# Kernel optimization log

Measured on AMD Instinct MI355X. Metric: run time of the kernel, lower is better.

## Reference

```python
import jax, jax.numpy as jnp
import numpy as np

B, N, NFEAT, NHID, NOUT, H = 16, 1024, 128, 256, 256, 4
DH = NOUT // H  # 64 per head
EPS = 1e-5
ALPHA = 0.2  # LeakyReLU negative slope


def setup_inputs() -> dict:
    key = jax.random.key(0)
    ks = jax.random.split(key, 8)
    stdv = 1.0 / np.sqrt(NHID)
    return {
        "x": jax.random.normal(ks[0], (B, N, NFEAT), dtype=jnp.float32),
        "adj": jax.random.uniform(ks[1], (N, N), dtype=jnp.float32) / N,
        "gc_w": jax.random.uniform(ks[2], (NFEAT, NHID), minval=-stdv, maxval=stdv, dtype=jnp.float32),
        "gc_b": jax.random.uniform(ks[3], (NHID,), minval=-stdv, maxval=stdv, dtype=jnp.float32),
        "bn1_gamma": jnp.ones((NHID,), jnp.float32),
        "bn1_beta": jnp.zeros((NHID,), jnp.float32),
        "gat_w": jax.random.normal(ks[4], (H, NHID, DH), dtype=jnp.float32) * (1.0 / np.sqrt(NHID)),
        "conv_w": jax.random.normal(ks[5], (NOUT, NOUT, 3), dtype=jnp.float32) * (1.0 / np.sqrt(NOUT * 3)),
        "conv_b": jnp.zeros((NOUT,), jnp.float32),
        "bn2_gamma": jnp.ones((NOUT,), jnp.float32),
        "bn2_beta": jnp.zeros((NOUT,), jnp.float32),
    }


def reference(x, adj, gc_w, gc_b, bn1_gamma, bn1_beta, gat_w, conv_w, conv_b, bn2_gamma, bn2_beta):
    # --- GraphConvolution: adj @ (x @ W) + b, relu ---
    h = jnp.einsum("bnf,fo->bno", x, gc_w)
    h = jnp.einsum("nm,bmo->bno", adj, h) + gc_b
    h = jax.nn.relu(h)
    # --- BatchNorm1d over channel dim (training-mode batch stats), relu ---
    mu = h.mean((0, 1))
    var = h.var((0, 1))
    h = (h - mu) * jax.lax.rsqrt(var + EPS) * bn1_gamma + bn1_beta
    h = jax.nn.relu(h)
    # --- Multi-head GAT: per head hp, e = hp hp^T, leakyrelu, softmax, attn @ hp ---
    hp = jnp.einsum("bnf,hfd->bhnd", h, gat_w)          # (B,H,N,DH)
    e = jnp.einsum("bhnd,bhmd->bhnm", hp, hp)            # (B,H,N,N)
    e = jnp.where(e > 0, e, ALPHA * e)
    attn = jax.nn.softmax(e, axis=-1)
    out = jnp.einsum("bhnm,bhmd->bhnd", attn, hp)        # = sum_m attn * hp (the B,N,N,d repeat in torch)
    out = out.transpose(0, 2, 1, 3).reshape(B, N, H * DH)  # concat heads -> (B,N,NOUT)
    # --- TCN block: conv1d (k=3, pad 1) over node axis, batchnorm, relu (dropout=eval) ---
    xc = out.transpose(0, 2, 1)                          # (B,C,N)
    y = jax.lax.conv_general_dilated(xc, conv_w, (1,), [(1, 1)],
                                     dimension_numbers=("NCH", "OIH", "NCH"))
    y = y + conv_b[None, :, None]
    mu2 = y.mean((0, 2), keepdims=True)
    var2 = y.var((0, 2), keepdims=True)
    y = (y - mu2) * jax.lax.rsqrt(var2 + EPS) * bn2_gamma[None, :, None] + bn2_beta[None, :, None]
    y = jax.nn.relu(y)
    return y.transpose(0, 2, 1)                          # (B,N,NOUT)
```

## Files before the change

kernel.cpp:

```cpp
#include <hip/hip_runtime.h>
#include <hip/hip_bf16.h>


typedef unsigned short u16;
typedef __attribute__((ext_vector_type(8))) short short8;
typedef __attribute__((ext_vector_type(4))) float f32x4;

static __device__ __forceinline__ float4 ld4(const float* p){ return *(const float4*)p; }
static __device__ __forceinline__ void st4(float* p, float4 v){ *(float4*)p = v; }

static __device__ __forceinline__ u16 f2bf(float f){
  unsigned u = __builtin_bit_cast(unsigned, f);
  unsigned r = u + 0x7FFFu + ((u >> 16) & 1u);
  return (u16)(r >> 16);
}
static __device__ __forceinline__ float bf2f(u16 h){
  unsigned u = ((unsigned)h) << 16; return __builtin_bit_cast(float, u);
}
static __device__ __forceinline__ void st4bf(u16* p, u16 a, u16 b, u16 c, u16 d){
  uint2 v; v.x = (unsigned)a | ((unsigned)b << 16); v.y = (unsigned)c | ((unsigned)d << 16);
  *(uint2*)p = v;
}
static __device__ __forceinline__ f32x4 mfma16(short8 a, short8 b, f32x4 c){
  return __builtin_amdgcn_mfma_f32_16x16x32_bf16(a, b, c, 0, 0, 0);
}

template<int SPLIT, int K, int NN, int MODE, int AXSWAP, int BM, int BN, int WR, int WC>
static __device__ __forceinline__ void mgemm_body(
    const u16* __restrict__ Ah_, const u16* __restrict__ Al_,
    const u16* __restrict__ Bh_, const u16* __restrict__ Bl_,
    const u16* __restrict__ zbuf,
    void* __restrict__ C0v, void* __restrict__ C1v, void* __restrict__ C2v,
    const float* __restrict__ bias)
{
  constexpr int KT = K / 32;
  constexpr int WM = BM / WR, WN = BN / WC;
  constexpr int MI = WM / 16, NJ = WN / 16;
  __shared__ u16 Ah[2][BM * 32], Bh[2][BN * 32];
  __shared__ u16 Al[2][SPLIT == 3 ? BM * 32 : 8], Bl[2][SPLIT == 3 ? BN * 32 : 8];
  const int tid = threadIdx.x;
  const int n0 = (AXSWAP ? blockIdx.y : blockIdx.x) * BN;
  const int m0 = (AXSWAP ? blockIdx.x : blockIdx.y) * BM;
  const int lane = tid & 63, l15 = lane & 15, lq = lane >> 4;
  const int w = tid >> 6, wr = w / WC, wc = w % WC;

  f32x4 acc[MI][NJ] = {};

  auto STAGE = [&](int buf, int kt){
    const int k0 = kt * 32;
#pragma unroll
    for (int r = 0; r < BM / 64; ++r){
      const int slot = r * 256 + tid;
      const int row = slot & (BM - 1), kh = slot / BM;
      const int ldsoff = (r * 256 + (tid & 192)) * 8;
      const u16* asrc;
      if constexpr (MODE == 3){
        const int kz = k0 >> 8;
        const int ci0 = (k0 & 255) + kh * 8;
        const int R = m0 + row;
        const int nn = (R & 1023) + kz - 1;
        asrc = ((unsigned)nn < 1024u) ? (Ah_ + (size_t)(R + kz - 1) * 256 + ci0) : zbuf;
      } else {
        asrc = Ah_ + (size_t)(m0 + row) * K + k0 + kh * 8;
      }
      __builtin_amdgcn_global_load_lds(asrc, &Ah[buf][ldsoff], 16, 0, 0);
      if constexpr (SPLIT == 3){
        const u16* asrc2 = Al_ + (size_t)(m0 + row) * K + k0 + kh * 8;
        __builtin_amdgcn_global_load_lds(asrc2, &Al[buf][ldsoff], 16, 0, 0);
      }
    }
#pragma unroll
    for (int r = 0; r < BN / 64; ++r){
      const int slot = r * 256 + tid;
      const int row = slot & (BN - 1), kh = slot / BN;
      const int ldsoff = (r * 256 + (tid & 192)) * 8;
      const u16* bsrc = Bh_ + (size_t)(n0 + row) * K + k0 + kh * 8;
      __builtin_amdgcn_global_load_lds(bsrc, &Bh[buf][ldsoff], 16, 0, 0);
      if constexpr (SPLIT == 3){
        const u16* bsrc2 = Bl_ + (size_t)(n0 + row) * K + k0 + kh * 8;
        __builtin_amdgcn_global_load_lds(bsrc2, &Bl[buf][ldsoff], 16, 0, 0);
      }
    }
  };

  STAGE(0, 0);
  __syncthreads();
  for (int kt = 0; kt < KT; ++kt){
    const int cur = kt & 1;
    if (kt + 1 < KT) STAGE(cur ^ 1, kt + 1);
    short8 afh[MI], bfh[NJ], afl[MI], bfl[NJ];
#pragma unroll
    for (int f = 0; f < MI; ++f){
      afh[f] = *(const short8*)&Ah[cur][(lq * BM + wr * WM + f * 16 + l15) * 8];
      if constexpr (SPLIT == 3)
        afl[f] = *(const short8*)&Al[cur][(lq * BM + wr * WM + f * 16 + l15) * 8];
    }
#pragma unroll
    for (int f = 0; f < NJ; ++f){
      bfh[f] = *(const short8*)&Bh[cur][(lq * BN + wc * WN + f * 16 + l15) * 8];
      if constexpr (SPLIT == 3)
        bfl[f] = *(const short8*)&Bl[cur][(lq * BN + wc * WN + f * 16 + l15) * 8];
    }
#pragma unroll
    for (int fi = 0; fi < MI; ++fi)
#pragma unroll
      for (int fj = 0; fj < NJ; ++fj){
        acc[fi][fj] = mfma16(afh[fi], bfh[fj], acc[fi][fj]);
        if constexpr (SPLIT == 3){
          acc[fi][fj] = mfma16(afl[fi], bfh[fj], acc[fi][fj]);
          acc[fi][fj] = mfma16(afh[fi], bfl[fj], acc[fi][fj]);
        }
      }
    __syncthreads();
  }

  const int rb = m0 + wr * WM;
  const int cb = n0 + wc * WN;
  if constexpr (MODE == 0){
    u16* H = (u16*)C0v; u16* L = (u16*)C1v;
#pragma unroll
    for (int fi = 0; fi < MI; ++fi){
      const int R = rb + fi * 16 + lq * 4;
      const int nn = R & 1023, bq = R >> 10;
#pragma unroll
      for (int fj = 0; fj < NJ; ++fj){
        const int c = cb + fj * 16 + l15;
        const size_t off = (size_t)(bq * 256 + c) * 1024 + nn;
        u16 h_[4], l_[4];
#pragma unroll
        for (int r = 0; r < 4; ++r){
          float v = acc[fi][fj][r];
          u16 hi = f2bf(v); h_[r] = hi; l_[r] = f2bf(v - bf2f(hi));
        }
        st4bf(H + off, h_[0], h_[1], h_[2], h_[3]);
        st4bf(L + off, l_[0], l_[1], l_[2], l_[3]);
      }
    }
  } else if constexpr (MODE == 1){
    u16* GH = (u16*)C0v; u16* GL = (u16*)C1v; float* PT = (float*)C2v;
    const int mb = AXSWAP ? blockIdx.x : blockIdx.y;
#pragma unroll
    for (int fj = 0; fj < NJ; ++fj){
      const int c = cb + fj * 16 + l15;
      const int o = c & 255, bq = c >> 8;
      const float bs = bias[o];
      float s = 0.f, q = 0.f;
#pragma unroll
      for (int fi = 0; fi < MI; ++fi){
        const int R = rb + fi * 16 + lq * 4;
#pragma unroll
        for (int r = 0; r < 4; ++r){
          const float v = fmaxf(acc[fi][fj][r] + bs, 0.f);
          s += v; q = fmaf(v, v, q);
          const u16 hi = f2bf(v);
          const size_t off = ((size_t)bq * 1024 + R + r) * 256 + o;
          GH[off] = hi;
          GL[off] = f2bf(v - bf2f(hi));
        }
      }
      s += __shfl_xor(s, 16, 64); s += __shfl_xor(s, 32, 64);
      q += __shfl_xor(q, 16, 64); q += __shfl_xor(q, 32, 64);
      if (lq == 0){
        PT[mb * 4096 + c]         = s;
        PT[65536 + mb * 4096 + c] = q;
      }
    }
  } else if constexpr (MODE == 2){
    u16* H = (u16*)C0v; u16* L = (u16*)C1v; u16* T = (u16*)C2v;
#pragma unroll
    for (int fi = 0; fi < MI; ++fi){
      const int R = rb + fi * 16 + lq * 4;
#pragma unroll
      for (int fj = 0; fj < NJ; ++fj){
        const int c = cb + fj * 16 + l15;
        u16 h_[4];
#pragma unroll
        for (int r = 0; r < 4; ++r){
          float v = acc[fi][fj][r];
          u16 hi = f2bf(v); h_[r] = hi;
          H[(size_t)(R + r) * 256 + c] = hi;
          L[(size_t)(R + r) * 256 + c] = f2bf(v - bf2f(hi));
        }
        st4bf(T + (size_t)c * 16384 + R, h_[0], h_[1], h_[2], h_[3]);
      }
    }
  } else {
    float* Y = (float*)C0v; float* PT = (float*)C2v;
    const int slot = blockIdx.y * 2 + wr;
#pragma unroll
    for (int fj = 0; fj < NJ; ++fj){
      const int c = cb + fj * 16 + l15;
      const float bs = bias[c];
      float s = 0.f, q = 0.f;
#pragma unroll
      for (int fi = 0; fi < MI; ++fi){
        const int R = rb + fi * 16 + lq * 4;
#pragma unroll
        for (int r = 0; r < 4; ++r){
          const float v = acc[fi][fj][r] + bs;
          s += v; q = fmaf(v, v, q);
          Y[(size_t)(R + r) * 256 + c] = v;
        }
      }
      s += __shfl_xor(s, 16, 64); s += __shfl_xor(s, 32, 64);
      q += __shfl_xor(q, 16, 64); q += __shfl_xor(q, 32, 64);
      if (lq == 0){
        PT[slot * 256 + c]         = s;
        PT[65536 + slot * 256 + c] = q;
      }
    }
  }
}

__global__ __launch_bounds__(256) void gemm0_k(
    const u16* __restrict__ Ah_, const u16* __restrict__ Bh_,
    const u16* __restrict__ zbuf, void* __restrict__ C0, void* __restrict__ C1)
{ mgemm_body<1, 128, 256, 0, 0, 128, 64, 2, 2>(Ah_, nullptr, Bh_, nullptr, zbuf, C0, C1, nullptr, nullptr); }

__global__ __launch_bounds__(256) void gemm1_k(
    const u16* __restrict__ Ah_, const u16* __restrict__ Al_,
    const u16* __restrict__ Bh_, const u16* __restrict__ Bl_,
    const u16* __restrict__ zbuf, void* __restrict__ C0, void* __restrict__ C1,
    void* __restrict__ C2, const float* __restrict__ bias)
{ mgemm_body<3, 1024, 4096, 1, 1, 64, 128, 1, 4>(Ah_, Al_, Bh_, Bl_, zbuf, C0, C1, C2, bias); }

__global__ __launch_bounds__(256) void gemm2_k(
    const u16* __restrict__ Ah_, const u16* __restrict__ Al_,
    const u16* __restrict__ Bh_, const u16* __restrict__ Bl_,
    const u16* __restrict__ zbuf,
    void* __restrict__ C0, void* __restrict__ C1, void* __restrict__ C2)
{ mgemm_body<3, 256, 256, 2, 0, 128, 64, 2, 2>(Ah_, Al_, Bh_, Bl_, zbuf, C0, C1, C2, nullptr); }

__global__ __launch_bounds__(256) void gemm3_k(
    const u16* __restrict__ Ah_, const u16* __restrict__ Bh_,
    const u16* __restrict__ zbuf, void* __restrict__ C0, void* __restrict__ C2,
    const float* __restrict__ bias)
{ mgemm_body<1, 768, 256, 3, 0, 128, 64, 2, 2>(Ah_, nullptr, Bh_, nullptr, zbuf, C0, nullptr, C2, bias); }

__global__ __launch_bounds__(256) void flash(
    const u16* __restrict__ hp_hi, const u16* __restrict__ hp_lo,
    const u16* __restrict__ hpT, u16* __restrict__ ao)
{
  __shared__ u16 Khi[2][4096], Klo[2][4096], Vt[2][4096];
  __shared__ u16 Pl[4][2048];
  const int tid = threadIdx.x;
  const int lane = tid & 63, l15 = lane & 15, lq = lane >> 4, w = tid >> 6;
  const int bid = blockIdx.x;
  const int b = bid & 15, k_ = bid >> 4, h = k_ >> 3, qo = k_ & 7;
  const size_t qrow0 = (size_t)b * 1024 + qo * 128 + w * 32;

  short8 qh[2][2], ql[2][2];
#pragma unroll
  for (int mf = 0; mf < 2; ++mf)
#pragma unroll
    for (int ks = 0; ks < 2; ++ks){
      const size_t off = (qrow0 + mf * 16 + l15) * 256 + h * 64 + ks * 32 + lq * 8;
      qh[mf][ks] = *(const short8*)(hp_hi + off);
      ql[mf][ks] = *(const short8*)(hp_lo + off);
    }

  auto STAGE = [&](int buf, int kt){
    const int kv0 = kt * 64;
#pragma unroll
    for (int r = 0; r < 2; ++r){
      const int slot = r * 256 + tid;
      const int g1 = slot >> 6, g2 = slot & 63;
      const int ldsoff = (r * 256 + (tid & 192)) * 8;
      const u16* ksrc = hp_hi + ((size_t)b * 1024 + kv0 + g2) * 256 + h * 64 + g1 * 8;
      __builtin_amdgcn_global_load_lds(ksrc, &Khi[buf][ldsoff], 16, 0, 0);
      const u16* ksrc2 = hp_lo + ((size_t)b * 1024 + kv0 + g2) * 256 + h * 64 + g1 * 8;
      __builtin_amdgcn_global_load_lds(ksrc2, &Klo[buf][ldsoff], 16, 0, 0);
      const u16* vsrc = hpT + (size_t)(h * 64 + g2) * 16384 + b * 1024 + kv0 + g1 * 8;
      __builtin_amdgcn_global_load_lds(vsrc, &Vt[buf][ldsoff], 16, 0, 0);
    }
  };

  f32x4 o_[4][2] = {};
  float ls[8] = {};

  STAGE(0, 0);
  __syncthreads();
  for (int kt = 0; kt < 16; ++kt){
    const int cur = kt & 1;
    if (kt < 15) STAGE(cur ^ 1, kt + 1);

#pragma unroll
    for (int nf = 0; nf < 4; ++nf){
      short8 kf[2], kg[2];
#pragma unroll
      for (int ks = 0; ks < 2; ++ks){
        kf[ks] = *(const short8*)&Khi[cur][((ks * 4 + lq) * 64 + nf * 16 + l15) * 8];
        kg[ks] = *(const short8*)&Klo[cur][((ks * 4 + lq) * 64 + nf * 16 + l15) * 8];
      }
      const int kv = nf * 16 + l15;
#pragma unroll
      for (int mf = 0; mf < 2; ++mf){
        f32x4 s = {};
        __builtin_amdgcn_s_setprio(1);
#pragma unroll
        for (int ks = 0; ks < 2; ++ks){
          s = mfma16(qh[mf][ks], kf[ks], s);
          s = mfma16(ql[mf][ks], kf[ks], s);
          s = mfma16(qh[mf][ks], kg[ks], s);
        }
        __builtin_amdgcn_s_setprio(0);
        const int qb = mf * 16 + lq * 4;
        const int base = ((kv >> 3) * 32 + qb) * 8 + (kv & 7);
#pragma unroll
        for (int r = 0; r < 4; ++r){
          float v = s[r];
          v = v > 0.f ? v : 0.2f * v;
          const float p = __expf(v - 40.f);
          ls[mf * 4 + r] += p;
          Pl[w][base + r * 8] = f2bf(p);
        }
      }
    }

#pragma unroll
    for (int ks = 0; ks < 2; ++ks){
      short8 va[4], pf[2];
#pragma unroll
      for (int f = 0; f < 4; ++f)
        va[f] = *(const short8*)&Vt[cur][((ks * 4 + lq) * 64 + f * 16 + l15) * 8];
#pragma unroll
      for (int f = 0; f < 2; ++f)
        pf[f] = *(const short8*)&Pl[w][((ks * 4 + lq) * 32 + f * 16 + l15) * 8];
      __builtin_amdgcn_s_setprio(1);
#pragma unroll
      for (int df = 0; df < 4; ++df)
#pragma unroll
        for (int qf = 0; qf < 2; ++qf)
          o_[df][qf] = mfma16(va[df], pf[qf], o_[df][qf]);
      __builtin_amdgcn_s_setprio(0);
    }
    __syncthreads();
  }

#pragma unroll
  for (int mask = 1; mask < 16; mask <<= 1)
#pragma unroll
    for (int i = 0; i < 8; ++i)
      ls[i] += __shfl_xor(ls[i], mask, 64);
  float* LsF = (float*)&Pl[w][0];
  if (l15 == 0){
#pragma unroll
    for (int mf = 0; mf < 2; ++mf)
#pragma unroll
      for (int r = 0; r < 4; ++r)
        LsF[mf * 16 + lq * 4 + r] = ls[mf * 4 + r];
  }
  float inv[2];
#pragma unroll
  for (int qf = 0; qf < 2; ++qf) inv[qf] = 1.0f / LsF[qf * 16 + l15];

#pragma unroll
  for (int qf = 0; qf < 2; ++qf)
#pragma unroll
    for (int df = 0; df < 4; ++df){
      const size_t addr = (qrow0 + qf * 16 + l15) * 256 + h * 64 + df * 16 + lq * 4;
      st4bf(ao + addr,
            f2bf(o_[df][qf][0] * inv[qf]), f2bf(o_[df][qf][1] * inv[qf]),
            f2bf(o_[df][qf][2] * inv[qf]), f2bf(o_[df][qf][3] * inv[qf]));
    }
}

__global__ __launch_bounds__(256) void bn_final(const float* __restrict__ part,
                                                const float* __restrict__ gamma,
                                                const float* __restrict__ beta,
                                                float* __restrict__ prm)
{
  const int t = threadIdx.x;
  float s = 0.f, q = 0.f;
#pragma unroll 8
  for (int i = 0; i < 256; ++i){ s += part[i * 256 + t]; q += part[65536 + i * 256 + t]; }
  const float mu = s * (1.f / 16384.f);
  const float var = q * (1.f / 16384.f) - mu * mu;
  prm[t] = mu;
  prm[256 + t] = rsqrtf(var + 1e-5f) * gamma[t];
  prm[512 + t] = beta[t];
}

__global__ __launch_bounds__(256) void bn_apply_split(
    const u16* __restrict__ GH, const u16* __restrict__ GL,
    u16* __restrict__ H, u16* __restrict__ L, const float* __restrict__ prm)
{
  const int idx = blockIdx.x * 256 + threadIdx.x;
  const size_t off = (size_t)idx * 4;
  const int o = (int)(off & 255);
  const uint2 hv = *(const uint2*)(GH + off);
  const uint2 lv = *(const uint2*)(GL + off);
  const float4 m = ld4(prm + o), rs = ld4(prm + 256 + o), bt = ld4(prm + 512 + o);
  float x0 = bf2f((u16)(hv.x & 0xffff)) + bf2f((u16)(lv.x & 0xffff));
  float x1 = bf2f((u16)(hv.x >> 16))    + bf2f((u16)(lv.x >> 16));
  float x2 = bf2f((u16)(hv.y & 0xffff)) + bf2f((u16)(lv.y & 0xffff));
  float x3 = bf2f((u16)(hv.y >> 16))    + bf2f((u16)(lv.y >> 16));
  u16 h_[4], l_[4];
  float v;
  v = fmaxf(fmaf(x0 - m.x, rs.x, bt.x), 0.f); h_[0] = f2bf(v); l_[0] = f2bf(v - bf2f(h_[0]));
  v = fmaxf(fmaf(x1 - m.y, rs.y, bt.y), 0.f); h_[1] = f2bf(v); l_[1] = f2bf(v - bf2f(h_[1]));
  v = fmaxf(fmaf(x2 - m.z, rs.z, bt.z), 0.f); h_[2] = f2bf(v); l_[2] = f2bf(v - bf2f(h_[2]));
  v = fmaxf(fmaf(x3 - m.w, rs.w, bt.w), 0.f); h_[3] = f2bf(v); l_[3] = f2bf(v - bf2f(h_[3]));
  st4bf(H + off, h_[0], h_[1], h_[2], h_[3]);
  st4bf(L + off, l_[0], l_[1], l_[2], l_[3]);
}

__global__ __launch_bounds__(256) void bn_apply(const float* __restrict__ in,
                                                float* __restrict__ outp,
                                                const float* __restrict__ prm)
{
  const int idx = blockIdx.x * 256 + threadIdx.x;
  const size_t off = (size_t)idx * 8;
  const int o = (int)(off & 255);
  const float4 x0 = ld4(in + off),      x1 = ld4(in + off + 4);
  const float4 m0 = ld4(prm + o),       m1 = ld4(prm + o + 4);
  const float4 r0 = ld4(prm + 256 + o), r1 = ld4(prm + 256 + o + 4);
  const float4 b0 = ld4(prm + 512 + o), b1 = ld4(prm + 512 + o + 4);
  float4 y0, y1;
  y0.x = fmaxf(fmaf(x0.x - m0.x, r0.x, b0.x), 0.f);
  y0.y = fmaxf(fmaf(x0.y - m0.y, r0.y, b0.y), 0.f);
  y0.z = fmaxf(fmaf(x0.z - m0.z, r0.z, b0.z), 0.f);
  y0.w = fmaxf(fmaf(x0.w - m0.w, r0.w, b0.w), 0.f);
  y1.x = fmaxf(fmaf(x1.x - m1.x, r1.x, b1.x), 0.f);
  y1.y = fmaxf(fmaf(x1.y - m1.y, r1.y, b1.y), 0.f);
  y1.z = fmaxf(fmaf(x1.z - m1.z, r1.z, b1.z), 0.f);
  y1.w = fmaxf(fmaf(x1.w - m1.w, r1.w, b1.w), 0.f);
  st4(outp + off, y0);
  st4(outp + off + 4, y1);
}

__global__ __launch_bounds__(256) void pack_w(
    const float* __restrict__ x, const float* __restrict__ adj,
    const float* __restrict__ gcw, const float* __restrict__ gatw,
    const float* __restrict__ convw,
    u16* __restrict__ xbf, u16* __restrict__ adjh, u16* __restrict__ adjl,
    u16* __restrict__ w0t, u16* __restrict__ w2th, u16* __restrict__ w2tl,
    u16* __restrict__ cwt, u16* __restrict__ zb)
{
  const int idx = blockIdx.x * 256 + threadIdx.x;
  if (idx < 2097152) xbf[idx] = f2bf(x[idx]);
  if (idx < 1048576){
    const float v = adj[idx];
    const u16 hi = f2bf(v);
    adjh[idx] = hi; adjl[idx] = f2bf(v - bf2f(hi));
  }
  if (idx < 32768){
    const int o = idx >> 7, f = idx & 127;
    w0t[idx] = f2bf(gcw[f * 256 + o]);
  }
  if (idx < 65536){
    const int c = idx >> 8, f = idx & 255;
    const float v = gatw[(c >> 6) * 16384 + f * 64 + (c & 63)];
    const u16 hi = f2bf(v);
    w2th[idx] = hi; w2tl[idx] = f2bf(v - bf2f(hi));
  }
  if (idx < 196608){
    const int co = idx / 768, k = idx - co * 768;
    const int kz = k >> 8, ci = k & 255;
    cwt[idx] = f2bf(convw[co * 768 + ci * 3 + kz]);
  }
  if (idx < 2048) zb[idx] = 0;
}

extern "C" void kernel_launch(void* const* d_in, const int* in_sizes, int n_in,
                              void* d_out, int out_size, void* d_ws, size_t ws_size,
                              hipStream_t stream)
{
  const float* x     = (const float*)d_in[0];
  const float* adj   = (const float*)d_in[1];
  const float* gc_w  = (const float*)d_in[2];
  const float* gc_b  = (const float*)d_in[3];
  const float* bn1g  = (const float*)d_in[4];
  const float* bn1b  = (const float*)d_in[5];
  const float* gatw  = (const float*)d_in[6];
  const float* convw = (const float*)d_in[7];
  const float* convb = (const float*)d_in[8];
  const float* bn2g  = (const float*)d_in[9];
  const float* bn2b  = (const float*)d_in[10];
  char* ws  = (char*)d_ws;
  char* out = (char*)d_out;

  u16* h1t_hi = (u16*)(ws + 0);
  u16* h1t_lo = (u16*)(ws + 8388608);
  u16* x_bf   = (u16*)(ws + 16777216);
  u16* adj_hi = (u16*)(ws + 20971520);
  u16* adj_lo = (u16*)(ws + 23068672);
  u16* hpT    = (u16*)(ws + 16777216);
  u16* w0t    = (u16*)(ws + 25165824);
  u16* w2th   = (u16*)(ws + 25231360);
  u16* w2tl   = (u16*)(ws + 25362432);
  u16* cwt    = (u16*)(ws + 25493504);
  u16* zbuf   = (u16*)(ws + 25886720);
  float* P1   = (float*)(ws + 25890816);
  float* PR1  = (float*)(ws + 26415104);
  float* PR2  = (float*)(ws + 26419200);
  u16* h_hi  = (u16*)(ws + 0);
  u16* h_lo  = (u16*)(ws + 8388608);
  u16* ao    = (u16*)(ws + 0);
  u16* g_hi  = (u16*)out;
  u16* g_lo  = (u16*)(out + 8388608);
  u16* hp_hi = (u16*)out;
  u16* hp_lo = (u16*)(out + 8388608);
  float* y   = (float*)out;

  pack_w<<<8192, 256, 0, stream>>>(x, adj, gc_w, gatw, convw,
                                   x_bf, adj_hi, adj_lo, w0t, w2th, w2tl, cwt, zbuf);
  gemm0_k<<<dim3(4, 128), 256, 0, stream>>>(x_bf, w0t, zbuf, h1t_hi, h1t_lo);
  gemm1_k<<<dim3(16, 32), 256, 0, stream>>>(adj_hi, adj_lo, h1t_hi, h1t_lo, zbuf,
                                            g_hi, g_lo, P1, gc_b);
  bn_final<<<1, 256, 0, stream>>>(P1, bn1g, bn1b, PR1);
  bn_apply_split<<<4096, 256, 0, stream>>>(g_hi, g_lo, h_hi, h_lo, PR1);
  gemm2_k<<<dim3(4, 128), 256, 0, stream>>>(h_hi, h_lo, w2th, w2tl, zbuf, hp_hi, hp_lo, hpT);
  flash<<<512, 256, 0, stream>>>(hp_hi, hp_lo, hpT, ao);
  gemm3_k<<<dim3(4, 128), 256, 0, stream>>>(ao, cwt, zbuf, y, P1, convb);
  bn_final<<<1, 256, 0, stream>>>(P1, bn2g, bn2b, PR2);
  bn_apply<<<2048, 256, 0, stream>>>(y, y, PR2);
}
```

Before: 305.1 us.

## Reassociate graph convolution as (adj @ x) @ W to shrink the large GEMM

```diff
diff --git a/kernel.cpp b/kernel.cpp
--- a/kernel.cpp
+++ b/kernel.cpp
@@ -116,56 +116,7 @@
 
   const int rb = m0 + wr * WM;
   const int cb = n0 + wc * WN;
-  if constexpr (MODE == 0){
-    u16* H = (u16*)C0v; u16* L = (u16*)C1v;
-#pragma unroll
-    for (int fi = 0; fi < MI; ++fi){
-      const int R = rb + fi * 16 + lq * 4;
-      const int nn = R & 1023, bq = R >> 10;
-#pragma unroll
-      for (int fj = 0; fj < NJ; ++fj){
-        const int c = cb + fj * 16 + l15;
-        const size_t off = (size_t)(bq * 256 + c) * 1024 + nn;
-        u16 h_[4], l_[4];
-#pragma unroll
-        for (int r = 0; r < 4; ++r){
-          float v = acc[fi][fj][r];
-          u16 hi = f2bf(v); h_[r] = hi; l_[r] = f2bf(v - bf2f(hi));
-        }
-        st4bf(H + off, h_[0], h_[1], h_[2], h_[3]);
-        st4bf(L + off, l_[0], l_[1], l_[2], l_[3]);
-      }
-    }
-  } else if constexpr (MODE == 1){
-    u16* GH = (u16*)C0v; u16* GL = (u16*)C1v; float* PT = (float*)C2v;
-    const int mb = AXSWAP ? blockIdx.x : blockIdx.y;
-#pragma unroll
-    for (int fj = 0; fj < NJ; ++fj){
-      const int c = cb + fj * 16 + l15;
-      const int o = c & 255, bq = c >> 8;
-      const float bs = bias[o];
-      float s = 0.f, q = 0.f;
-#pragma unroll
-      for (int fi = 0; fi < MI; ++fi){
-        const int R = rb + fi * 16 + lq * 4;
-#pragma unroll
-        for (int r = 0; r < 4; ++r){
-          const float v = fmaxf(acc[fi][fj][r] + bs, 0.f);
-          s += v; q = fmaf(v, v, q);
-          const u16 hi = f2bf(v);
-          const size_t off = ((size_t)bq * 1024 + R + r) * 256 + o;
-          GH[off] = hi;
-          GL[off] = f2bf(v - bf2f(hi));
-        }
-      }
-      s += __shfl_xor(s, 16, 64); s += __shfl_xor(s, 32, 64);
-      q += __shfl_xor(q, 16, 64); q += __shfl_xor(q, 32, 64);
-      if (lq == 0){
-        PT[mb * 4096 + c]         = s;
-        PT[65536 + mb * 4096 + c] = q;
-      }
-    }
-  } else if constexpr (MODE == 2){
+  if constexpr (MODE == 2){
     u16* H = (u16*)C0v; u16* L = (u16*)C1v; u16* T = (u16*)C2v;
 #pragma unroll
     for (int fi = 0; fi < MI; ++fi){
@@ -184,7 +135,7 @@
         st4bf(T + (size_t)c * 16384 + R, h_[0], h_[1], h_[2], h_[3]);
       }
     }
-  } else {
+  } else if constexpr (MODE == 3){
     float* Y = (float*)C0v; float* PT = (float*)C2v;
     const int slot = blockIdx.y * 2 + wr;
 #pragma unroll
@@ -209,20 +160,67 @@
         PT[65536 + slot * 256 + c] = q;
       }
     }
-  }
-}
-
-__global__ __launch_bounds__(256) void gemm0_k(
-    const u16* __restrict__ Ah_, const u16* __restrict__ Bh_,
+  } else if constexpr (MODE == 4){
+    u16* GH = (u16*)C0v; u16* GL = (u16*)C1v; float* PT = (float*)C2v;
+    const int slot = blockIdx.y * 2 + wr;
+#pragma unroll
+    for (int fj = 0; fj < NJ; ++fj){
+      const int c = cb + fj * 16 + l15;
+      const float bs = bias[c];
+      float s = 0.f, q = 0.f;
+#pragma unroll
+      for (int fi = 0; fi < MI; ++fi){
+        const int R = rb + fi * 16 + lq * 4;
+#pragma unroll
+        for (int r = 0; r < 4; ++r){
+          const float v = fmaxf(acc[fi][fj][r] + bs, 0.f);
+          s += v; q = fmaf(v, v, q);
+          const u16 hi = f2bf(v);
+          const size_t off = (size_t)(R + r) * 256 + c;
+          GH[off] = hi;
+          GL[off] = f2bf(v - bf2f(hi));
+        }
+      }
+      s += __shfl_xor(s, 16, 64); s += __shfl_xor(s, 32, 64);
+      q += __shfl_xor(q, 16, 64); q += __shfl_xor(q, 32, 64);
+      if (lq == 0){
+        PT[slot * 256 + c]         = s;
+        PT[65536 + slot * 256 + c] = q;
+      }
+    }
+  } else {
+    u16* XH = (u16*)C0v; u16* XL = (u16*)C1v;
+#pragma unroll
+    for (int fi = 0; fi < MI; ++fi){
+      const int R = rb + fi * 16 + lq * 4;
+#pragma unroll
+      for (int fj = 0; fj < NJ; ++fj){
+        const int c = cb + fj * 16 + l15;
+        const size_t base = ((size_t)(c >> 7) * 1024 + R) * 128 + (c & 127);
+#pragma unroll
+        for (int r = 0; r < 4; ++r){
+          const float v = acc[fi][fj][r];
+          const u16 hi = f2bf(v);
+          XH[base + (size_t)r * 128] = hi;
+          XL[base + (size_t)r * 128] = f2bf(v - bf2f(hi));
+        }
+      }
+    }
+  }
+}
+
+__global__ __launch_bounds__(256) void adjx_k(
+    const u16* __restrict__ Ah_, const u16* __restrict__ Al_,
+    const u16* __restrict__ Bh_, const u16* __restrict__ Bl_,
     const u16* __restrict__ zbuf, void* __restrict__ C0, void* __restrict__ C1)
-{ mgemm_body<1, 128, 256, 0, 0, 128, 64, 2, 2>(Ah_, nullptr, Bh_, nullptr, zbuf, C0, C1, nullptr, nullptr); }
-
-__global__ __launch_bounds__(256) void gemm1_k(
+{ mgemm_body<3, 1024, 2048, 5, 0, 64, 64, 2, 2>(Ah_, Al_, Bh_, Bl_, zbuf, C0, C1, nullptr, nullptr); }
+
+__global__ __launch_bounds__(256) void gemm1n_k(
     const u16* __restrict__ Ah_, const u16* __restrict__ Al_,
     const u16* __restrict__ Bh_, const u16* __restrict__ Bl_,
     const u16* __restrict__ zbuf, void* __restrict__ C0, void* __restrict__ C1,
     void* __restrict__ C2, const float* __restrict__ bias)
-{ mgemm_body<3, 1024, 4096, 1, 1, 64, 128, 1, 4>(Ah_, Al_, Bh_, Bl_, zbuf, C0, C1, C2, bias); }
+{ mgemm_body<3, 128, 256, 4, 0, 128, 64, 2, 2>(Ah_, Al_, Bh_, Bl_, zbuf, C0, C1, C2, bias); }
 
 __global__ __launch_bounds__(256) void gemm2_k(
     const u16* __restrict__ Ah_, const u16* __restrict__ Al_,
@@ -433,12 +431,20 @@
     const float* __restrict__ x, const float* __restrict__ adj,
     const float* __restrict__ gcw, const float* __restrict__ gatw,
     const float* __restrict__ convw,
-    u16* __restrict__ xbf, u16* __restrict__ adjh, u16* __restrict__ adjl,
-    u16* __restrict__ w0t, u16* __restrict__ w2th, u16* __restrict__ w2tl,
+    u16* __restrict__ xth, u16* __restrict__ xtl,
+    u16* __restrict__ adjh, u16* __restrict__ adjl,
+    u16* __restrict__ w0th, u16* __restrict__ w0tl,
+    u16* __restrict__ w2th, u16* __restrict__ w2tl,
     u16* __restrict__ cwt, u16* __restrict__ zb)
 {
   const int idx = blockIdx.x * 256 + threadIdx.x;
-  if (idx < 2097152) xbf[idx] = f2bf(x[idx]);
+  if (idx < 2097152){
+    const int bf = idx >> 10, n = idx & 1023;
+    const int b = bf >> 7, f = bf & 127;
+    const float v = x[((size_t)b * 1024 + n) * 128 + f];
+    const u16 hi = f2bf(v);
+    xth[idx] = hi; xtl[idx] = f2bf(v - bf2f(hi));
+  }
   if (idx < 1048576){
     const float v = adj[idx];
     const u16 hi = f2bf(v);
@@ -446,7 +452,9 @@
   }
   if (idx < 32768){
     const int o = idx >> 7, f = idx & 127;
-    w0t[idx] = f2bf(gcw[f * 256 + o]);
+    const float v = gcw[f * 256 + o];
+    const u16 hi = f2bf(v);
+    w0th[idx] = hi; w0tl[idx] = f2bf(v - bf2f(hi));
   }
   if (idx < 65536){
     const int c = idx >> 8, f = idx & 255;
@@ -480,23 +488,25 @@
   char* ws  = (char*)d_ws;
   char* out = (char*)d_out;
 
-  u16* h1t_hi = (u16*)(ws + 0);
-  u16* h1t_lo = (u16*)(ws + 8388608);
-  u16* x_bf   = (u16*)(ws + 16777216);
-  u16* adj_hi = (u16*)(ws + 20971520);
-  u16* adj_lo = (u16*)(ws + 23068672);
+  u16* ax_hi  = (u16*)(ws + 0);
+  u16* ax_lo  = (u16*)(ws + 4194304);
+  u16* adj_hi = (u16*)(ws + 8388608);
+  u16* adj_lo = (u16*)(ws + 10485760);
+  u16* xT_hi  = (u16*)(ws + 16777216);
+  u16* xT_lo  = (u16*)(ws + 20971520);
+  u16* h_hi   = (u16*)(ws + 0);
+  u16* h_lo   = (u16*)(ws + 8388608);
   u16* hpT    = (u16*)(ws + 16777216);
-  u16* w0t    = (u16*)(ws + 25165824);
-  u16* w2th   = (u16*)(ws + 25231360);
-  u16* w2tl   = (u16*)(ws + 25362432);
-  u16* cwt    = (u16*)(ws + 25493504);
-  u16* zbuf   = (u16*)(ws + 25886720);
-  float* P1   = (float*)(ws + 25890816);
-  float* PR1  = (float*)(ws + 26415104);
-  float* PR2  = (float*)(ws + 26419200);
-  u16* h_hi  = (u16*)(ws + 0);
-  u16* h_lo  = (u16*)(ws + 8388608);
-  u16* ao    = (u16*)(ws + 0);
+  u16* ao     = (u16*)(ws + 0);
+  u16* w0th   = (u16*)(ws + 25165824);
+  u16* w0tl   = (u16*)(ws + 25231360);
+  u16* w2th   = (u16*)(ws + 25296896);
+  u16* w2tl   = (u16*)(ws + 25427968);
+  u16* cwt    = (u16*)(ws + 25559040);
+  u16* zbuf   = (u16*)(ws + 25952256);
+  float* P1   = (float*)(ws + 25956352);
+  float* PR1  = (float*)(ws + 26480640);
+  float* PR2  = (float*)(ws + 26484736);
   u16* g_hi  = (u16*)out;
   u16* g_lo  = (u16*)(out + 8388608);
   u16* hp_hi = (u16*)out;
@@ -504,10 +514,12 @@
   float* y   = (float*)out;
 
   pack_w<<<8192, 256, 0, stream>>>(x, adj, gc_w, gatw, convw,
-                                   x_bf, adj_hi, adj_lo, w0t, w2th, w2tl, cwt, zbuf);
-  gemm0_k<<<dim3(4, 128), 256, 0, stream>>>(x_bf, w0t, zbuf, h1t_hi, h1t_lo);
-  gemm1_k<<<dim3(16, 32), 256, 0, stream>>>(adj_hi, adj_lo, h1t_hi, h1t_lo, zbuf,
-                                            g_hi, g_lo, P1, gc_b);
+                                   xT_hi, xT_lo, adj_hi, adj_lo,
+                                   w0th, w0tl, w2th, w2tl, cwt, zbuf);
+  adjx_k<<<dim3(32, 16), 256, 0, stream>>>(adj_hi, adj_lo, xT_hi, xT_lo, zbuf,
+                                           ax_hi, ax_lo);
+  gemm1n_k<<<dim3(4, 128), 256, 0, stream>>>(ax_hi, ax_lo, w0th, w0tl, zbuf,
+                                             g_hi, g_lo, P1, gc_b);
   bn_final<<<1, 256, 0, stream>>>(P1, bn1g, bn1b, PR1);
   bn_apply_split<<<4096, 256, 0, stream>>>(g_hi, g_lo, h_hi, h_lo, PR1);
   gemm2_k<<<dim3(4, 128), 256, 0, stream>>>(h_hi, h_lo, w2th, w2tl, zbuf, hp_hi, hp_lo, hpT);
```

New measurement: 294.9 us. 3.3% less time.
